# Performance work log

Hardware: AMD Instinct MI355X
Metric: run time of the kernel (lower is better)

The kernel has to match this reference:

```python
import jax, jax.numpy as jnp
import numpy as np

BATCH, N_AGENTS, OBS_DIM, ACTOR_DIM, N_ACTIONS = 8192, 64, 128, 64, 32


def setup_inputs() -> dict:
    key = jax.random.key(0)
    ks = jax.random.split(key, 14)
    s = 0.05
    inp = {
        "O": jax.random.normal(ks[0], (BATCH, N_AGENTS, OBS_DIM), dtype=jnp.float32),
        "W_enc": jax.random.normal(ks[1], (OBS_DIM, ACTOR_DIM), dtype=jnp.float32) * s,
        "b_enc": jax.random.normal(ks[2], (ACTOR_DIM,), dtype=jnp.float32) * s,
        "W1": jax.random.normal(ks[3], (2 * ACTOR_DIM, ACTOR_DIM), dtype=jnp.float32) * s,
        "b1": jax.random.normal(ks[4], (ACTOR_DIM,), dtype=jnp.float32) * s,
        "W2": jax.random.normal(ks[5], (2 * ACTOR_DIM, ACTOR_DIM), dtype=jnp.float32) * s,
        "b2": jax.random.normal(ks[6], (ACTOR_DIM,), dtype=jnp.float32) * s,
        "W3": jax.random.normal(ks[7], (2 * ACTOR_DIM, ACTOR_DIM), dtype=jnp.float32) * s,
        "b3": jax.random.normal(ks[8], (ACTOR_DIM,), dtype=jnp.float32) * s,
        "W4": jax.random.normal(ks[9], (2 * ACTOR_DIM, ACTOR_DIM), dtype=jnp.float32) * s,
        "b4": jax.random.normal(ks[10], (ACTOR_DIM,), dtype=jnp.float32) * s,
        "W_dec": jax.random.normal(ks[11], (N_AGENTS * ACTOR_DIM, N_ACTIONS), dtype=jnp.float32) * s,
        "b_dec": jax.random.normal(ks[12], (N_ACTIONS,), dtype=jnp.float32) * s,
    }
    return inp


def _comm_layer(H, W, b, n_agents):
    # get_commvar: masked mean over other agents, but divided by n_agents
    # (the zeroed self term is included in the mean denominator) ->
    # C_i = (sum_j H_j - H_i) / n_agents, exactly equal to the original math.
    C = (jnp.sum(H, axis=1, keepdims=True) - H) / n_agents  # [B, A, D]
    Hcat = jnp.concatenate([H, C], axis=-1)                 # [B, A, 2D]
    return Hcat @ W + b                                     # no activation (faithful)


def reference(O, W_enc, b_enc, W1, b1, W2, b2, W3, b3, W4, b4, W_dec, b_dec):
    B, A, _ = O.shape
    H = jax.nn.sigmoid(O @ W_enc + b_enc)  # [B, A, D]
    H = _comm_layer(H, W1, b1, A)
    H = _comm_layer(H, W2, b2, A)
    H = _comm_layer(H, W3, b3, A)
    H = _comm_layer(H, W4, b4, A)
    Hf = H.reshape(B, -1)                  # [B, A*D]
    return Hf @ W_dec + b_dec              # [B, n_actions]
```

## Files before the change

kernel.cpp:

```cpp
#include <hip/hip_runtime.h>
#include <stdint.h>


#define BATCHN 8192
#define NAGENT 64
#define OBSD   128
#define DD     64
#define NACT   32

typedef __attribute__((ext_vector_type(8))) short short8;
typedef __attribute__((ext_vector_type(4))) float floatx4;

__device__ __forceinline__ unsigned short f2b(float f) {
    union { float f; uint32_t u; } v; v.f = f;
    uint32_t r = v.u + 0x7FFFu + ((v.u >> 16) & 1u);
    return (unsigned short)(r >> 16);
}

#define OFF_WENC 0
#define OFF_WCAT 16384
#define OFF_WDEC 81920
#define OFF_H4   344064

__global__ __launch_bounds__(256) void prep_kernel(
    const float* __restrict__ Wenc,
    const float* __restrict__ W1, const float* __restrict__ W2,
    const float* __restrict__ W3, const float* __restrict__ W4,
    const float* __restrict__ Wdec,
    unsigned short* __restrict__ ws)
{
    int tid = blockIdx.x * 256 + threadIdx.x;
    if (tid < 8192) {
        int n = tid >> 7, k = tid & 127;
        ws[OFF_WENC/2 + n*128 + k] = f2b(Wenc[k*64 + n]);
    } else if (tid < 5*8192) {
        int l = (tid - 8192) >> 13;
        int e = (tid - 8192) & 8191;
        int n = e >> 7, k = e & 127;
        const float* W = (l==0) ? W1 : (l==1) ? W2 : (l==2) ? W3 : W4;
        float v = W[k*64 + n];
        if (k < 64) v -= W[(k+64)*64 + n] * (1.0f/64.0f);
        ws[OFF_WCAT/2 + l*8192 + n*128 + k] = f2b(v);
    } else {
        int e = tid - 5*8192;
        int n = e >> 12, k = e & 4095;
        ws[OFF_WDEC/2 + n*4096 + k] = f2b(Wdec[k*32 + n]);
    }
}

__global__ __launch_bounds__(256) void fused_kernel(
    const float* __restrict__ O,
    const unsigned short* __restrict__ WencT,
    const unsigned short* __restrict__ WcatT,
    const float* __restrict__ b_enc,
    const float* __restrict__ b1, const float* __restrict__ b2,
    const float* __restrict__ b3, const float* __restrict__ b4,
    unsigned short* __restrict__ H4out)
{
    __shared__ __align__(16) unsigned short sA[64*136];
    __shared__ __align__(16) unsigned short sW[64*136];
    __shared__ __align__(16) unsigned short sH[64*72];
    __shared__ __align__(16) unsigned short sS[64];
    __shared__ float sPart[4][64];

    const int t = threadIdx.x;
    const int b = blockIdx.x;
    const int lane = t & 63;
    const int w = t >> 6;
    const int m = lane & 15;
    const int q = lane >> 4;

    {
        const float* Ob = O + (size_t)b * (NAGENT*OBSD);
        #pragma unroll
        for (int i = 0; i < 8; i++) {
            int e = t*4 + i*1024;
            float4 f = *(const float4*)(Ob + e);
            int row = e >> 7, col = e & 127;
            uint2 pk;
            pk.x = (uint32_t)f2b(f.x) | ((uint32_t)f2b(f.y) << 16);
            pk.y = (uint32_t)f2b(f.z) | ((uint32_t)f2b(f.w) << 16);
            *(uint2*)&sA[row*136 + col] = pk;
        }
        #pragma unroll
        for (int i = 0; i < 4; i++) {
            int c = t + i*256;
            int e = c*8;
            int row = e >> 7, col = e & 127;
            *(uint4*)&sW[row*136 + col] = *(const uint4*)(WencT + e);
        }
    }
    __syncthreads();

    floatx4 acc[4];

    #pragma unroll
    for (int nt = 0; nt < 4; nt++) {
        float bias = b_enc[nt*16 + m];
        acc[nt] = (floatx4){bias, bias, bias, bias};
    }
    #pragma unroll
    for (int s = 0; s < 4; s++) {
        short8 a = *(const short8*)&sA[(w*16 + m)*136 + s*32 + q*8];
        #pragma unroll
        for (int nt = 0; nt < 4; nt++) {
            short8 bb = *(const short8*)&sW[(nt*16 + m)*136 + s*32 + q*8];
            acc[nt] = __builtin_amdgcn_mfma_f32_16x16x32_bf16(a, bb, acc[nt], 0, 0, 0);
        }
    }
    #pragma unroll
    for (int nt = 0; nt < 4; nt++)
        #pragma unroll
        for (int r = 0; r < 4; r++)
            acc[nt][r] = 1.0f / (1.0f + __expf(-acc[nt][r]));

    #pragma unroll
    for (int nt = 0; nt < 4; nt++) {
        float s = acc[nt][0] + acc[nt][1] + acc[nt][2] + acc[nt][3];
        s += __shfl_xor(s, 16, 64);
        s += __shfl_xor(s, 32, 64);
        if (q == 0) sPart[w][nt*16 + m] = s;
        #pragma unroll
        for (int r = 0; r < 4; r++)
            sH[(w*16 + q*4 + r)*72 + nt*16 + m] = f2b(acc[nt][r]);
    }

    const float* bs[4] = {b1, b2, b3, b4};
    #pragma unroll
    for (int l = 0; l < 4; l++) {
        __syncthreads();
        #pragma unroll
        for (int i = 0; i < 4; i++) {
            int c = t + i*256;
            int e = c*8;
            int row = e >> 7, col = e & 127;
            *(uint4*)&sW[row*136 + col] = *(const uint4*)(WcatT + l*8192 + e);
        }
        if (t < 64)
            sS[t] = f2b((sPart[0][t] + sPart[1][t] + sPart[2][t] + sPart[3][t]) * (1.0f/64.0f));
        __syncthreads();

        const float* bl = bs[l];
        #pragma unroll
        for (int nt = 0; nt < 4; nt++) {
            float bias = bl[nt*16 + m];
            acc[nt] = (floatx4){bias, bias, bias, bias};
        }
        #pragma unroll
        for (int s = 0; s < 2; s++) {
            short8 a = *(const short8*)&sH[(w*16 + m)*72 + s*32 + q*8];
            #pragma unroll
            for (int nt = 0; nt < 4; nt++) {
                short8 bb = *(const short8*)&sW[(nt*16 + m)*136 + s*32 + q*8];
                acc[nt] = __builtin_amdgcn_mfma_f32_16x16x32_bf16(a, bb, acc[nt], 0, 0, 0);
            }
        }
        #pragma unroll
        for (int s = 0; s < 2; s++) {
            short8 a = *(const short8*)&sS[s*32 + q*8];
            #pragma unroll
            for (int nt = 0; nt < 4; nt++) {
                short8 bb = *(const short8*)&sW[(nt*16 + m)*136 + (s+2)*32 + q*8];
                acc[nt] = __builtin_amdgcn_mfma_f32_16x16x32_bf16(a, bb, acc[nt], 0, 0, 0);
            }
        }

        if (l < 3) {
            #pragma unroll
            for (int nt = 0; nt < 4; nt++) {
                float s = acc[nt][0] + acc[nt][1] + acc[nt][2] + acc[nt][3];
                s += __shfl_xor(s, 16, 64);
                s += __shfl_xor(s, 32, 64);
                if (q == 0) sPart[w][nt*16 + m] = s;
                #pragma unroll
                for (int r = 0; r < 4; r++)
                    sH[(w*16 + q*4 + r)*72 + nt*16 + m] = f2b(acc[nt][r]);
            }
        } else {
            unsigned short* Hb = H4out + (size_t)b * 4096;
            #pragma unroll
            for (int nt = 0; nt < 4; nt++)
                #pragma unroll
                for (int r = 0; r < 4; r++)
                    Hb[(w*16 + q*4 + r)*64 + nt*16 + m] = f2b(acc[nt][r]);
        }
    }
}

__global__ __launch_bounds__(512) void dec_kernel(
    const unsigned short* __restrict__ Hf,
    const unsigned short* __restrict__ WdecT,
    const float* __restrict__ b_dec,
    float* __restrict__ out)
{
    __shared__ float red[8][16][34];
    const int t = threadIdx.x;
    const int wv = t >> 6, lane = t & 63;
    const int m = lane & 15, q = lane >> 4;
    const int rb = blockIdx.x;
    const int kc = wv;

    const unsigned short* aP  = Hf    + (size_t)(rb*16 + m)*4096 + kc*512 + q*8;
    const unsigned short* bP0 = WdecT + (size_t)m*4096        + kc*512 + q*8;
    const unsigned short* bP1 = WdecT + (size_t)(16 + m)*4096 + kc*512 + q*8;

    floatx4 a0 = {0.f, 0.f, 0.f, 0.f}, a1 = {0.f, 0.f, 0.f, 0.f};
    #pragma unroll 4
    for (int s = 0; s < 16; s++) {
        short8 av  = *(const short8*)(aP  + s*32);
        short8 b0v = *(const short8*)(bP0 + s*32);
        short8 b1v = *(const short8*)(bP1 + s*32);
        a0 = __builtin_amdgcn_mfma_f32_16x16x32_bf16(av, b0v, a0, 0, 0, 0);
        a1 = __builtin_amdgcn_mfma_f32_16x16x32_bf16(av, b1v, a1, 0, 0, 0);
    }
    #pragma unroll
    for (int r = 0; r < 4; r++) {
        red[wv][q*4 + r][m]      = a0[r];
        red[wv][q*4 + r][16 + m] = a1[r];
    }
    __syncthreads();
    const int row = t >> 5, col = t & 31;
    float sum = b_dec[col];
    #pragma unroll
    for (int i = 0; i < 8; i++)
        sum += red[i][row][col];
    out[(size_t)(rb*16 + row)*32 + col] = sum;
}

extern "C" void kernel_launch(void* const* d_in, const int* in_sizes, int n_in,
                              void* d_out, int out_size, void* d_ws, size_t ws_size,
                              hipStream_t stream)
{
    const float* O    = (const float*)d_in[0];
    const float* Wenc = (const float*)d_in[1];
    const float* benc = (const float*)d_in[2];
    const float* W1   = (const float*)d_in[3];
    const float* b1   = (const float*)d_in[4];
    const float* W2   = (const float*)d_in[5];
    const float* b2   = (const float*)d_in[6];
    const float* W3   = (const float*)d_in[7];
    const float* b3   = (const float*)d_in[8];
    const float* W4   = (const float*)d_in[9];
    const float* b4   = (const float*)d_in[10];
    const float* Wdec = (const float*)d_in[11];
    const float* bdec = (const float*)d_in[12];
    float* out = (float*)d_out;
    unsigned short* ws = (unsigned short*)d_ws;

    prep_kernel<<<672, 256, 0, stream>>>(Wenc, W1, W2, W3, W4, Wdec, ws);
    fused_kernel<<<BATCHN, 256, 0, stream>>>(O, ws + OFF_WENC/2, ws + OFF_WCAT/2,
                                             benc, b1, b2, b3, b4, ws + OFF_H4/2);
    dec_kernel<<<512, 512, 0, stream>>>(ws + OFF_H4/2, ws + OFF_WDEC/2, bdec, out);
}
```

Baseline: 453.1 us.

## Load O and weight fragments directly from global into MFMA registers, drop LDS staging

Removes the shared-memory staging buffers for the observation tile and weight matrices. Each lane now loads its MFMA A fragments straight from global O, converting to bf16 in registers, and reads B fragments directly from the global bf16 weight arrays, which should hit in cache. This cuts LDS usage sharply, removes one barrier and the per-layer weight copy. A launch-bounds occupancy hint of 6 is added to exploit the freed LDS. The cost is redundant global/L2 reads of weights across waves and less coalesced O loads.

```diff
diff --git a/kernel.cpp b/kernel.cpp
--- a/kernel.cpp
+++ b/kernel.cpp
@@ -48,7 +48,7 @@
     }
 }
 
-__global__ __launch_bounds__(256) void fused_kernel(
+__global__ __launch_bounds__(256, 6) void fused_kernel(
     const float* __restrict__ O,
     const unsigned short* __restrict__ WencT,
     const unsigned short* __restrict__ WcatT,
@@ -57,8 +57,6 @@
     const float* __restrict__ b3, const float* __restrict__ b4,
     unsigned short* __restrict__ H4out)
 {
-    __shared__ __align__(16) unsigned short sA[64*136];
-    __shared__ __align__(16) unsigned short sW[64*136];
     __shared__ __align__(16) unsigned short sH[64*72];
     __shared__ __align__(16) unsigned short sS[64];
     __shared__ float sPart[4][64];
@@ -70,28 +68,6 @@
     const int m = lane & 15;
     const int q = lane >> 4;
 
-    {
-        const float* Ob = O + (size_t)b * (NAGENT*OBSD);
-        #pragma unroll
-        for (int i = 0; i < 8; i++) {
-            int e = t*4 + i*1024;
-            float4 f = *(const float4*)(Ob + e);
-            int row = e >> 7, col = e & 127;
-            uint2 pk;
-            pk.x = (uint32_t)f2b(f.x) | ((uint32_t)f2b(f.y) << 16);
-            pk.y = (uint32_t)f2b(f.z) | ((uint32_t)f2b(f.w) << 16);
-            *(uint2*)&sA[row*136 + col] = pk;
-        }
-        #pragma unroll
-        for (int i = 0; i < 4; i++) {
-            int c = t + i*256;
-            int e = c*8;
-            int row = e >> 7, col = e & 127;
-            *(uint4*)&sW[row*136 + col] = *(const uint4*)(WencT + e);
-        }
-    }
-    __syncthreads();
-
     floatx4 acc[4];
 
     #pragma unroll
@@ -99,13 +75,23 @@
         float bias = b_enc[nt*16 + m];
         acc[nt] = (floatx4){bias, bias, bias, bias};
     }
-    #pragma unroll
-    for (int s = 0; s < 4; s++) {
-        short8 a = *(const short8*)&sA[(w*16 + m)*136 + s*32 + q*8];
-        #pragma unroll
-        for (int nt = 0; nt < 4; nt++) {
-            short8 bb = *(const short8*)&sW[(nt*16 + m)*136 + s*32 + q*8];
-            acc[nt] = __builtin_amdgcn_mfma_f32_16x16x32_bf16(a, bb, acc[nt], 0, 0, 0);
+    {
+        const float* Ob = O + (size_t)b * (NAGENT*OBSD) + (w*16 + m)*OBSD + q*8;
+        #pragma unroll
+        for (int s = 0; s < 4; s++) {
+            float4 f0 = *(const float4*)(Ob + s*32);
+            float4 f1 = *(const float4*)(Ob + s*32 + 4);
+            union { short8 s8; unsigned short u[8]; } ua;
+            ua.u[0] = f2b(f0.x); ua.u[1] = f2b(f0.y);
+            ua.u[2] = f2b(f0.z); ua.u[3] = f2b(f0.w);
+            ua.u[4] = f2b(f1.x); ua.u[5] = f2b(f1.y);
+            ua.u[6] = f2b(f1.z); ua.u[7] = f2b(f1.w);
+            short8 a = ua.s8;
+            #pragma unroll
+            for (int nt = 0; nt < 4; nt++) {
+                short8 bb = *(const short8*)(WencT + (nt*16 + m)*128 + s*32 + q*8);
+                acc[nt] = __builtin_amdgcn_mfma_f32_16x16x32_bf16(a, bb, acc[nt], 0, 0, 0);
+            }
         }
     }
     #pragma unroll
@@ -129,17 +115,11 @@
     #pragma unroll
     for (int l = 0; l < 4; l++) {
         __syncthreads();
-        #pragma unroll
-        for (int i = 0; i < 4; i++) {
-            int c = t + i*256;
-            int e = c*8;
-            int row = e >> 7, col = e & 127;
-            *(uint4*)&sW[row*136 + col] = *(const uint4*)(WcatT + l*8192 + e);
-        }
         if (t < 64)
             sS[t] = f2b((sPart[0][t] + sPart[1][t] + sPart[2][t] + sPart[3][t]) * (1.0f/64.0f));
         __syncthreads();
 
+        const unsigned short* Wl = WcatT + l*8192;
         const float* bl = bs[l];
         #pragma unroll
         for (int nt = 0; nt < 4; nt++) {
@@ -151,7 +131,7 @@
             short8 a = *(const short8*)&sH[(w*16 + m)*72 + s*32 + q*8];
             #pragma unroll
             for (int nt = 0; nt < 4; nt++) {
-                short8 bb = *(const short8*)&sW[(nt*16 + m)*136 + s*32 + q*8];
+                short8 bb = *(const short8*)(Wl + (nt*16 + m)*128 + s*32 + q*8);
                 acc[nt] = __builtin_amdgcn_mfma_f32_16x16x32_bf16(a, bb, acc[nt], 0, 0, 0);
             }
         }
@@ -160,7 +140,7 @@
             short8 a = *(const short8*)&sS[s*32 + q*8];
             #pragma unroll
             for (int nt = 0; nt < 4; nt++) {
-                short8 bb = *(const short8*)&sW[(nt*16 + m)*136 + (s+2)*32 + q*8];
+                short8 bb = *(const short8*)(Wl + (nt*16 + m)*128 + (s+2)*32 + q*8);
                 acc[nt] = __builtin_amdgcn_mfma_f32_16x16x32_bf16(a, bb, acc[nt], 0, 0, 0);
             }
         }
```

Measured after the change: 636.0 us. 40.4% more time.
